# Optimization experiments

Measured on AMD Instinct MI355X. Metric: run time of the kernel, lower is better.

Reference implementation:

```python
import jax, jax.numpy as jnp
import numpy as np

EPS_POOL = 1e-9
NEG_INF = -1e9
TEMPERATURE = 0.07


def _l2norm(x, axis=-1, eps=1e-12):
    # matches torch F.normalize(p=2): x / max(||x||, eps)
    n = jnp.sqrt(jnp.sum(x * x, axis=axis, keepdims=True))
    return x / jnp.maximum(n, eps)


def setup_inputs() -> dict:
    key = jax.random.key(0)
    ks = jax.random.split(key, 8)
    B, Lq, Lc, D = 256, 128, 512, 384
    question_tokens = jax.random.normal(ks[0], (B, Lq, D), dtype=jnp.float32)
    chunk_tokens = jax.random.normal(ks[1], (B, Lc, D), dtype=jnp.float32)
    q_mask = jax.random.randint(ks[2], (B, Lq), 0, 2, dtype=jnp.int32)
    c_mask = jax.random.randint(ks[3], (B, Lc), 0, 2, dtype=jnp.int32)
    # ensure at least one valid token per row (avoid fully-masked rows)
    q_mask = q_mask.at[:, 0].set(1)
    c_mask = c_mask.at[:, 0].set(1)
    W1 = jax.random.normal(ks[4], (D, D), dtype=jnp.float32) * (1.0 / np.sqrt(D))
    b1 = jnp.zeros((D,), dtype=jnp.float32)
    W2 = jax.random.normal(ks[5], (D, D), dtype=jnp.float32) * (1.0 / np.sqrt(D))
    b2 = jnp.zeros((D,), dtype=jnp.float32)
    return {"question_tokens": question_tokens, "chunk_tokens": chunk_tokens,
            "q_mask": q_mask, "c_mask": c_mask,
            "W1": W1, "b1": b1, "W2": W2, "b2": b2}


def _encode(tokens, mask, W1, b1, W2, b2):
    # mean pool over valid tokens: [B,L,D] -> [B,D]
    m = mask.astype(tokens.dtype)[..., None]
    pooled = jnp.sum(tokens * m, axis=1) / jnp.maximum(jnp.sum(m, axis=1), EPS_POOL)
    h = jax.nn.relu(pooled @ W1 + b1)
    proj = h @ W2 + b2
    return _l2norm(proj, axis=1)


def _late_interaction(q_tokens, c_tokens, q_mask, c_mask):
    qn = _l2norm(q_tokens)                      # [B,Lq,D]
    cn = _l2norm(c_tokens)                      # [B,Lc,D]
    sims = jnp.einsum('bqd,bkd->bqk', qn, cn)   # [B,Lq,Lc]
    valid = q_mask[:, :, None].astype(bool) & c_mask[:, None, :].astype(bool)
    sims = jnp.where(valid, sims, NEG_INF)
    max_sim = jnp.max(sims, axis=-1)            # [B,Lq]
    max_sim = jnp.where(q_mask.astype(bool), max_sim, 0.0)
    return jnp.sum(max_sim, axis=-1)            # [B]


def reference(question_tokens, chunk_tokens, q_mask, c_mask, W1, b1, W2, b2):
    q_emb = _encode(question_tokens, q_mask, W1, b1, W2, b2)  # [B,D]
    c_emb = _encode(chunk_tokens, c_mask, W1, b1, W2, b2)     # [B,D]
    contrastive_sim = (q_emb @ c_emb.T) / TEMPERATURE         # [B,B]
    late_sim = _late_interaction(question_tokens, chunk_tokens, q_mask, c_mask)  # [B]
    return contrastive_sim, late_sim
```

## Files before the change

kernel.cpp:

```cpp
#include <hip/hip_runtime.h>
#include <hip/hip_bf16.h>
#include <stdint.h>

#define NB 256
#define LQ 128
#define LC 512
#define DIM 384
#define TCD 32
#define QP 392

typedef __attribute__((ext_vector_type(8))) short short8;
typedef __attribute__((ext_vector_type(4))) float f32x4;

__device__ __forceinline__ unsigned short f2bf(float x) {
  union { float f; uint32_t u; } c; c.f = x;
  return (unsigned short)((c.u + 0x7fffu + ((c.u >> 16) & 1u)) >> 16);
}

__global__ __launch_bounds__(512, 1)
void fused_pool_late(const float* __restrict__ qtok, const float* __restrict__ ctok,
                     const int* __restrict__ qm, const int* __restrict__ cm,
                     float* __restrict__ pooled, float* __restrict__ late) {
  __shared__ unsigned short s_q[LQ][QP];
  __shared__ unsigned short s_c[TCD][QP];
  __shared__ float s_pq[8][DIM];
  __shared__ float s_pc[8][DIM];
  __shared__ float s_cnt[2][8];
  __shared__ int   s_cval[TCD];
  __shared__ float s_wsum[8];

  const int b = blockIdx.x;
  const int tid = threadIdx.x;
  const int wave = tid >> 6;
  const int lane = tid & 63;
  const int rA = lane & 15;
  const int kof = (lane >> 4) * 8;

  const float* qb = qtok + (size_t)b * LQ * DIM;
  const float* cb = ctok + (size_t)b * LC * DIM;
  const int* qmb = qm + b * LQ;
  const int* cmb = cm + b * LC;

  float pq[6] = {0.f,0.f,0.f,0.f,0.f,0.f};
  float cq = 0.f;
  for (int r0 = 0; r0 < 16; ++r0) {
    const int r = wave * 16 + r0;
    const float* src = qb + r * DIM;
    float v[6], ss = 0.f;
#pragma unroll
    for (int j = 0; j < 6; ++j) { v[j] = src[lane + 64 * j]; ss += v[j] * v[j]; }
#pragma unroll
    for (int o = 32; o; o >>= 1) ss += __shfl_xor(ss, o);
    const float inv = 1.0f / fmaxf(sqrtf(ss), 1e-12f);
    const float fm = (float)qmb[r];
#pragma unroll
    for (int j = 0; j < 6; ++j) {
      s_q[r][lane + 64 * j] = f2bf(v[j] * inv);
      pq[j] = fmaf(v[j], fm, pq[j]);
    }
    cq += fm;
  }
#pragma unroll
  for (int j = 0; j < 6; ++j) s_pq[wave][lane + 64 * j] = pq[j];
  if (lane == 0) s_cnt[0][wave] = cq;

  float rm[4] = {-1e9f, -1e9f, -1e9f, -1e9f};
  float pc[6] = {0.f,0.f,0.f,0.f,0.f,0.f};
  float cc = 0.f;

  for (int t = 0; t < LC / TCD; ++t) {
    __syncthreads();
#pragma unroll
    for (int r0 = 0; r0 < 4; ++r0) {
      const int r = wave * 4 + r0;
      const int crow = t * TCD + r;
      const float* src = cb + crow * DIM;
      float v[6], ss = 0.f;
#pragma unroll
      for (int j = 0; j < 6; ++j) { v[j] = src[lane + 64 * j]; ss += v[j] * v[j]; }
#pragma unroll
      for (int o = 32; o; o >>= 1) ss += __shfl_xor(ss, o);
      const float inv = 1.0f / fmaxf(sqrtf(ss), 1e-12f);
      const int mk = cmb[crow];
      const float fm = (float)mk;
#pragma unroll
      for (int j = 0; j < 6; ++j) {
        s_c[r][lane + 64 * j] = f2bf(v[j] * inv);
        pc[j] = fmaf(v[j], fm, pc[j]);
      }
      cc += fm;
      if (lane == 0) s_cval[r] = mk;
    }
    __syncthreads();

    const unsigned short* ap  = &s_q[wave * 16 + rA][kof];
    const unsigned short* bp0 = &s_c[rA][kof];
    const unsigned short* bp1 = &s_c[rA + 16][kof];
    f32x4 acc0 = {0.f,0.f,0.f,0.f};
    f32x4 acc1 = {0.f,0.f,0.f,0.f};
#pragma unroll
    for (int kk = 0; kk < 12; ++kk) {
      short8 a  = *(const short8*)(ap  + kk * 32);
      short8 b0 = *(const short8*)(bp0 + kk * 32);
      short8 b1 = *(const short8*)(bp1 + kk * 32);
      acc0 = __builtin_amdgcn_mfma_f32_16x16x32_bf16(a, b0, acc0, 0, 0, 0);
      acc1 = __builtin_amdgcn_mfma_f32_16x16x32_bf16(a, b1, acc1, 0, 0, 0);
    }
    const bool v0 = s_cval[rA] != 0;
    const bool v1 = s_cval[rA + 16] != 0;
#pragma unroll
    for (int r = 0; r < 4; ++r) {
      const float a0 = v0 ? acc0[r] : -1e9f;
      const float a1 = v1 ? acc1[r] : -1e9f;
      rm[r] = fmaxf(rm[r], fmaxf(a0, a1));
    }
  }

#pragma unroll
  for (int j = 0; j < 6; ++j) s_pc[wave][lane + 64 * j] = pc[j];
  if (lane == 0) s_cnt[1][wave] = cc;

#pragma unroll
  for (int r = 0; r < 4; ++r) {
#pragma unroll
    for (int o = 1; o < 16; o <<= 1) rm[r] = fmaxf(rm[r], __shfl_xor(rm[r], o));
  }
  float ps = 0.f;
  if (rA == 0) {
    const int rowb = wave * 16 + (lane >> 4) * 4;
#pragma unroll
    for (int r = 0; r < 4; ++r) ps += qmb[rowb + r] ? rm[r] : 0.f;
  }
#pragma unroll
  for (int o = 32; o; o >>= 1) ps += __shfl_xor(ps, o);
  if (lane == 0) s_wsum[wave] = ps;
  __syncthreads();

  if (tid < DIM) {
    float sq = 0.f, sc = 0.f, nq = 0.f, nc = 0.f;
#pragma unroll
    for (int w = 0; w < 8; ++w) {
      sq += s_pq[w][tid];
      sc += s_pc[w][tid];
      nq += s_cnt[0][w];
      nc += s_cnt[1][w];
    }
    pooled[b * DIM + tid] = sq / fmaxf(nq, 1e-9f);
    pooled[(NB + b) * DIM + tid] = sc / fmaxf(nc, 1e-9f);
  }
  if (tid == 0) {
    float tot = 0.f;
#pragma unroll
    for (int w = 0; w < 8; ++w) tot += s_wsum[w];
    late[b] = tot;
  }
}

__global__ __launch_bounds__(DIM)
void mlp_kernel(const float* __restrict__ pooled,
                const float* __restrict__ W1, const float* __restrict__ b1,
                const float* __restrict__ W2, const float* __restrict__ b2,
                float* __restrict__ emb) {
  __shared__ float s_in[DIM];
  __shared__ float s_h[DIM];
  __shared__ float s_red[6];
  const int row = blockIdx.y * NB + blockIdx.x;
  const int d = threadIdx.x;
  s_in[d] = pooled[row * DIM + d];
  __syncthreads();
  float acc = b1[d];
#pragma unroll 8
  for (int k = 0; k < DIM; ++k) acc = fmaf(s_in[k], W1[k * DIM + d], acc);
  s_h[d] = fmaxf(acc, 0.f);
  __syncthreads();
  float p = b2[d];
#pragma unroll 8
  for (int k = 0; k < DIM; ++k) p = fmaf(s_h[k], W2[k * DIM + d], p);
  float ss = p * p;
#pragma unroll
  for (int o = 32; o; o >>= 1) ss += __shfl_xor(ss, o);
  if ((d & 63) == 0) s_red[d >> 6] = ss;
  __syncthreads();
  float tot = 0.f;
#pragma unroll
  for (int w = 0; w < 6; ++w) tot += s_red[w];
  emb[row * DIM + d] = p * (1.0f / fmaxf(sqrtf(tot), 1e-12f));
}

__global__ __launch_bounds__(NB)
void contrast_kernel(const float* __restrict__ emb, float* __restrict__ out0) {
  __shared__ float s_q[DIM];
  const int i = blockIdx.x;
  for (int k = threadIdx.x; k < DIM; k += NB) s_q[k] = emb[i * DIM + k];
  __syncthreads();
  const float* ce = emb + (size_t)(NB + threadIdx.x) * DIM;
  float acc = 0.f;
#pragma unroll 8
  for (int k = 0; k < DIM; ++k) acc = fmaf(s_q[k], ce[k], acc);
  out0[i * NB + threadIdx.x] = acc / 0.07f;
}

extern "C" void kernel_launch(void* const* d_in, const int* in_sizes, int n_in,
                              void* d_out, int out_size, void* d_ws, size_t ws_size,
                              hipStream_t stream) {
  const float* qtok = (const float*)d_in[0];
  const float* ctok = (const float*)d_in[1];
  const int*   qmm  = (const int*)d_in[2];
  const int*   cmm  = (const int*)d_in[3];
  const float* W1   = (const float*)d_in[4];
  const float* b1   = (const float*)d_in[5];
  const float* W2   = (const float*)d_in[6];
  const float* b2   = (const float*)d_in[7];

  float* out0 = (float*)d_out;
  float* late = out0 + NB * NB;
  float* pooled = (float*)d_ws;
  float* emb    = pooled + 2 * NB * DIM;

  hipLaunchKernelGGL(fused_pool_late, dim3(NB), dim3(512), 0, stream,
                     qtok, ctok, qmm, cmm, pooled, late);
  hipLaunchKernelGGL(mlp_kernel, dim3(NB, 2), dim3(DIM), 0, stream,
                     pooled, W1, b1, W2, b2, emb);
  hipLaunchKernelGGL(contrast_kernel, dim3(NB), dim3(NB), 0, stream, emb, out0);
}
```

Before: 134.7 us.

## Double-buffer token loads via async global-to-LDS and batch rows in MLP/contrast

The fused pooling/late-interaction kernel now streams query and chunk tiles into double-buffered LDS with global_load_lds, using an XOR swizzle, so global loads overlap the normalisation and MFMA work. Token rows are converted to bf16 unnormalised, and the per-row inverse norms are applied to the MFMA outputs afterwards. Query A-fragments are kept in registers across all chunk tiles. The MLP kernel now processes 4 rows per block and the contrastive kernel 8 rows per block, so weight and embedding loads are reused across rows. This adds LDS pressure and relies on hand-placed waitcnt and barrier code; bf16 rounding of unnormalised values slightly changes numerics.

```diff
diff --git a/kernel.cpp b/kernel.cpp
--- a/kernel.cpp
+++ b/kernel.cpp
@@ -6,119 +6,165 @@
 #define LQ 128
 #define LC 512
 #define DIM 384
-#define TCD 32
-#define QP 392
+#define TROWS 32
+#define ROW_BYTES (DIM * 4)
+#define STAGE_BYTES (TROWS * ROW_BYTES)
+#define NSTAGE 20
+#define CBP 392
 
 typedef __attribute__((ext_vector_type(8))) short short8;
-typedef __attribute__((ext_vector_type(4))) float f32x4;
-
-__device__ __forceinline__ unsigned short f2bf(float x) {
-  union { float f; uint32_t u; } c; c.f = x;
-  return (unsigned short)((c.u + 0x7fffu + ((c.u >> 16) & 1u)) >> 16);
+typedef __attribute__((ext_vector_type(4))) float f4;
+typedef __attribute__((ext_vector_type(2))) unsigned int u32x2;
+
+__device__ __forceinline__ unsigned int pk2bf(float a, float b) {
+  union { float f; uint32_t u; } x, y; x.f = a; y.f = b;
+  uint32_t lo = (x.u + 0x7fffu + ((x.u >> 16) & 1u)) >> 16;
+  uint32_t hi = (y.u + 0x7fffu + ((y.u >> 16) & 1u)) >> 16;
+  return lo | (hi << 16);
+}
+
+__device__ __forceinline__ void gload16(const void* g, void* l) {
+  __builtin_amdgcn_global_load_lds(
+      (const __attribute__((address_space(1))) void*)g,
+      (__attribute__((address_space(3))) void*)l, 16, 0, 0);
+}
+
+__device__ __forceinline__ void bar_lgkm() {
+  asm volatile("s_waitcnt lgkmcnt(0)" ::: "memory");
+  __builtin_amdgcn_s_barrier();
+  __builtin_amdgcn_sched_barrier(0);
 }
 
 __global__ __launch_bounds__(512, 1)
 void fused_pool_late(const float* __restrict__ qtok, const float* __restrict__ ctok,
                      const int* __restrict__ qm, const int* __restrict__ cm,
                      float* __restrict__ pooled, float* __restrict__ late) {
-  __shared__ unsigned short s_q[LQ][QP];
-  __shared__ unsigned short s_c[TCD][QP];
-  __shared__ float s_pq[8][DIM];
-  __shared__ float s_pc[8][DIM];
-  __shared__ float s_cnt[2][8];
-  __shared__ int   s_cval[TCD];
+  __shared__ float fbuf[2][TROWS * DIM];
+  __shared__ unsigned short s_cb[TROWS][CBP];
+  __shared__ float s_qinv[LQ];
+  __shared__ float s_cinv[TROWS];
+  __shared__ int s_qm[LQ];
+  __shared__ int s_cm[LC];
+  __shared__ float s_cnt[16];
   __shared__ float s_wsum[8];
 
   const int b = blockIdx.x;
   const int tid = threadIdx.x;
-  const int wave = tid >> 6;
-  const int lane = tid & 63;
-  const int rA = lane & 15;
-  const int kof = (lane >> 4) * 8;
-
-  const float* qb = qtok + (size_t)b * LQ * DIM;
-  const float* cb = ctok + (size_t)b * LC * DIM;
-  const int* qmb = qm + b * LQ;
-  const int* cmb = cm + b * LC;
-
-  float pq[6] = {0.f,0.f,0.f,0.f,0.f,0.f};
-  float cq = 0.f;
-  for (int r0 = 0; r0 < 16; ++r0) {
-    const int r = wave * 16 + r0;
-    const float* src = qb + r * DIM;
-    float v[6], ss = 0.f;
-#pragma unroll
-    for (int j = 0; j < 6; ++j) { v[j] = src[lane + 64 * j]; ss += v[j] * v[j]; }
-#pragma unroll
-    for (int o = 32; o; o >>= 1) ss += __shfl_xor(ss, o);
-    const float inv = 1.0f / fmaxf(sqrtf(ss), 1e-12f);
-    const float fm = (float)qmb[r];
-#pragma unroll
-    for (int j = 0; j < 6; ++j) {
-      s_q[r][lane + 64 * j] = f2bf(v[j] * inv);
-      pq[j] = fmaf(v[j], fm, pq[j]);
-    }
-    cq += fm;
-  }
-#pragma unroll
-  for (int j = 0; j < 6; ++j) s_pq[wave][lane + 64 * j] = pq[j];
-  if (lane == 0) s_cnt[0][wave] = cq;
-
+  const int wave = tid >> 6, lane = tid & 63;
+  const int rA = lane & 15, hi = lane >> 4;
+
+  const char* qb = (const char*)(qtok + (size_t)b * LQ * DIM);
+  const char* cb = (const char*)(ctok + (size_t)b * LC * DIM);
+
+  if (tid < LQ) s_qm[tid] = qm[b * LQ + tid];
+  s_cm[tid] = cm[b * LC + tid];
+  __syncthreads();
+
+  int goff[6];
+#pragma unroll
+  for (int j = 0; j < 6; ++j) {
+    unsigned n = (unsigned)wave * 384u + (unsigned)j * 64u + (unsigned)lane;
+    unsigned row = n / 96u, cc = n % 96u;
+    goff[j] = (int)(row * ROW_BYTES + ((cc ^ (row & 7u)) << 4));
+  }
+
+  {
+    char* ldst = (char*)&fbuf[0][0] + wave * 6144;
+#pragma unroll
+    for (int j = 0; j < 6; ++j) gload16(qb + goff[j], ldst + j * 1024);
+  }
+
+  f4 pqa = {0.f,0.f,0.f,0.f}, pqb = {0.f,0.f,0.f,0.f};
+  f4 pca = {0.f,0.f,0.f,0.f}, pcb = {0.f,0.f,0.f,0.f};
+  float cq = 0.f, ccnt = 0.f;
   float rm[4] = {-1e9f, -1e9f, -1e9f, -1e9f};
-  float pc[6] = {0.f,0.f,0.f,0.f,0.f,0.f};
-  float cc = 0.f;
-
-  for (int t = 0; t < LC / TCD; ++t) {
-    __syncthreads();
+  short8 A[12] = {};
+
+  for (int t = 0; t < NSTAGE; ++t) {
+    const int cur = t & 1;
+    if (t + 1 < NSTAGE) {
+      const char* base = (t + 1 < 4) ? (qb + (size_t)(t + 1) * STAGE_BYTES)
+                                     : (cb + (size_t)(t + 1 - 4) * STAGE_BYTES);
+      char* ldst = (char*)&fbuf[cur ^ 1][0] + wave * 6144;
+#pragma unroll
+      for (int j = 0; j < 6; ++j) gload16(base + goff[j], ldst + j * 1024);
+      asm volatile("s_waitcnt vmcnt(6)" ::: "memory");
+    } else {
+      asm volatile("s_waitcnt vmcnt(0)" ::: "memory");
+    }
+    __builtin_amdgcn_sched_barrier(0);
+
+    const char* fb = (const char*)&fbuf[cur][0];
+    const bool isq = (t < 4);
 #pragma unroll
     for (int r0 = 0; r0 < 4; ++r0) {
-      const int r = wave * 4 + r0;
-      const int crow = t * TCD + r;
-      const float* src = cb + crow * DIM;
-      float v[6], ss = 0.f;
-#pragma unroll
-      for (int j = 0; j < 6; ++j) { v[j] = src[lane + 64 * j]; ss += v[j] * v[j]; }
+      const int lrow = wave * 4 + r0;
+      const int k7 = lrow & 7;
+      const f4 va = *(const f4*)(fb + lrow * ROW_BYTES + ((lane ^ k7) << 4));
+      f4 vb = {0.f,0.f,0.f,0.f};
+      if (lane < 32) vb = *(const f4*)(fb + lrow * ROW_BYTES + (((64 + lane) ^ k7) << 4));
+      float ss = va.x*va.x + va.y*va.y + va.z*va.z + va.w*va.w
+               + vb.x*vb.x + vb.y*vb.y + vb.z*vb.z + vb.w*vb.w;
 #pragma unroll
       for (int o = 32; o; o >>= 1) ss += __shfl_xor(ss, o);
       const float inv = 1.0f / fmaxf(sqrtf(ss), 1e-12f);
-      const int mk = cmb[crow];
+      const int mk = isq ? s_qm[t * 32 + lrow] : s_cm[(t - 4) * 32 + lrow];
       const float fm = (float)mk;
-#pragma unroll
-      for (int j = 0; j < 6; ++j) {
-        s_c[r][lane + 64 * j] = f2bf(v[j] * inv);
-        pc[j] = fmaf(v[j], fm, pc[j]);
-      }
-      cc += fm;
-      if (lane == 0) s_cval[r] = mk;
-    }
-    __syncthreads();
-
-    const unsigned short* ap  = &s_q[wave * 16 + rA][kof];
-    const unsigned short* bp0 = &s_c[rA][kof];
-    const unsigned short* bp1 = &s_c[rA + 16][kof];
-    f32x4 acc0 = {0.f,0.f,0.f,0.f};
-    f32x4 acc1 = {0.f,0.f,0.f,0.f};
-#pragma unroll
-    for (int kk = 0; kk < 12; ++kk) {
-      short8 a  = *(const short8*)(ap  + kk * 32);
-      short8 b0 = *(const short8*)(bp0 + kk * 32);
-      short8 b1 = *(const short8*)(bp1 + kk * 32);
-      acc0 = __builtin_amdgcn_mfma_f32_16x16x32_bf16(a, b0, acc0, 0, 0, 0);
-      acc1 = __builtin_amdgcn_mfma_f32_16x16x32_bf16(a, b1, acc1, 0, 0, 0);
-    }
-    const bool v0 = s_cval[rA] != 0;
-    const bool v1 = s_cval[rA + 16] != 0;
-#pragma unroll
-    for (int r = 0; r < 4; ++r) {
-      const float a0 = v0 ? acc0[r] : -1e9f;
-      const float a1 = v1 ? acc1[r] : -1e9f;
-      rm[r] = fmaxf(rm[r], fmaxf(a0, a1));
-    }
-  }
-
-#pragma unroll
-  for (int j = 0; j < 6; ++j) s_pc[wave][lane + 64 * j] = pc[j];
-  if (lane == 0) s_cnt[1][wave] = cc;
+      if (isq) {
+        pqa += va * fm; pqb += vb * fm; cq += fm;
+        if (lane == 0) s_qinv[t * 32 + lrow] = inv;
+      } else {
+        pca += va * fm; pcb += vb * fm; ccnt += fm;
+        if (lane == 0) s_cinv[lrow] = inv;
+      }
+      u32x2 w0; w0[0] = pk2bf(va.x, va.y); w0[1] = pk2bf(va.z, va.w);
+      *(u32x2*)&s_cb[lrow][4 * lane] = w0;
+      if (lane < 32) {
+        u32x2 w1; w1[0] = pk2bf(vb.x, vb.y); w1[1] = pk2bf(vb.z, vb.w);
+        *(u32x2*)&s_cb[lrow][256 + 4 * lane] = w1;
+      }
+    }
+    bar_lgkm();
+
+    if (isq) {
+      if ((wave >> 1) == t) {
+        const int lbase = (wave & 1) * 16 + rA;
+#pragma unroll
+        for (int kk = 0; kk < 12; ++kk)
+          A[kk] = *(const short8*)&s_cb[lbase][kk * 32 + hi * 8];
+        asm volatile("s_waitcnt lgkmcnt(0)" ::: "memory");
+        __builtin_amdgcn_sched_barrier(0);
+      }
+    } else {
+      f4 acc0 = {0.f,0.f,0.f,0.f}, acc1 = {0.f,0.f,0.f,0.f};
+#pragma unroll
+      for (int kk = 0; kk < 12; ++kk) {
+        const short8 b0 = *(const short8*)&s_cb[rA][kk * 32 + hi * 8];
+        const short8 b1 = *(const short8*)&s_cb[rA + 16][kk * 32 + hi * 8];
+        acc0 = __builtin_amdgcn_mfma_f32_16x16x32_bf16(A[kk], b0, acc0, 0, 0, 0);
+        acc1 = __builtin_amdgcn_mfma_f32_16x16x32_bf16(A[kk], b1, acc1, 0, 0, 0);
+      }
+      const int tb = (t - 4) * 32;
+      const bool v0 = s_cm[tb + rA] != 0;
+      const bool v1 = s_cm[tb + rA + 16] != 0;
+      const float ci0 = s_cinv[rA], ci1 = s_cinv[rA + 16];
+#pragma unroll
+      for (int r = 0; r < 4; ++r) {
+        const float qi = s_qinv[wave * 16 + hi * 4 + r];
+        const float a0 = v0 ? acc0[r] * (qi * ci0) : -1e9f;
+        const float a1 = v1 ? acc1[r] * (qi * ci1) : -1e9f;
+        rm[r] = fmaxf(rm[r], fmaxf(a0, a1));
+      }
+    }
+    bar_lgkm();
+  }
+
+  float* red = (float*)&fbuf[0][0];
+  *(f4*)&red[wave * DIM + 4 * lane] = pqa;
+  if (lane < 32) *(f4*)&red[wave * DIM + 256 + 4 * lane] = pqb;
+  *(f4*)&red[(8 + wave) * DIM + 4 * lane] = pca;
+  if (lane < 32) *(f4*)&red[(8 + wave) * DIM + 256 + 4 * lane] = pcb;
+  if (lane == 0) { s_cnt[wave] = cq; s_cnt[8 + wave] = ccnt; }
 
 #pragma unroll
   for (int r = 0; r < 4; ++r) {
@@ -127,9 +173,9 @@
   }
   float ps = 0.f;
   if (rA == 0) {
-    const int rowb = wave * 16 + (lane >> 4) * 4;
-#pragma unroll
-    for (int r = 0; r < 4; ++r) ps += qmb[rowb + r] ? rm[r] : 0.f;
+    const int rowb = wave * 16 + hi * 4;
+#pragma unroll
+    for (int r = 0; r < 4; ++r) ps += s_qm[rowb + r] ? rm[r] : 0.f;
   }
 #pragma unroll
   for (int o = 32; o; o >>= 1) ps += __shfl_xor(ps, o);
@@ -140,10 +186,10 @@
     float sq = 0.f, sc = 0.f, nq = 0.f, nc = 0.f;
 #pragma unroll
     for (int w = 0; w < 8; ++w) {
-      sq += s_pq[w][tid];
-      sc += s_pc[w][tid];
-      nq += s_cnt[0][w];
-      nc += s_cnt[1][w];
+      sq += red[w * DIM + tid];
+      sc += red[(8 + w) * DIM + tid];
+      nq += s_cnt[w];
+      nc += s_cnt[8 + w];
     }
     pooled[b * DIM + tid] = sq / fmaxf(nq, 1e-9f);
     pooled[(NB + b) * DIM + tid] = sc / fmaxf(nc, 1e-9f);
@@ -157,47 +203,68 @@
 }
 
 __global__ __launch_bounds__(DIM)
-void mlp_kernel(const float* __restrict__ pooled,
-                const float* __restrict__ W1, const float* __restrict__ b1,
-                const float* __restrict__ W2, const float* __restrict__ b2,
-                float* __restrict__ emb) {
-  __shared__ float s_in[DIM];
-  __shared__ float s_h[DIM];
-  __shared__ float s_red[6];
-  const int row = blockIdx.y * NB + blockIdx.x;
+void mlp_kernel(const float* __restrict__ pooled, const float* __restrict__ W1,
+                const float* __restrict__ b1, const float* __restrict__ W2,
+                const float* __restrict__ b2, float* __restrict__ emb) {
+  __shared__ float s_in[4][DIM];
+  __shared__ float s_h[4][DIM];
+  __shared__ float s_red[4][6];
+  const int r0 = blockIdx.x * 4;
   const int d = threadIdx.x;
-  s_in[d] = pooled[row * DIM + d];
-  __syncthreads();
-  float acc = b1[d];
+#pragma unroll
+  for (int r = 0; r < 4; ++r) s_in[r][d] = pooled[(size_t)(r0 + r) * DIM + d];
+  __syncthreads();
+  float acc[4] = {b1[d], b1[d], b1[d], b1[d]};
 #pragma unroll 8
-  for (int k = 0; k < DIM; ++k) acc = fmaf(s_in[k], W1[k * DIM + d], acc);
-  s_h[d] = fmaxf(acc, 0.f);
-  __syncthreads();
-  float p = b2[d];
+  for (int k = 0; k < DIM; ++k) {
+    const float w = W1[k * DIM + d];
+#pragma unroll
+    for (int r = 0; r < 4; ++r) acc[r] = fmaf(s_in[r][k], w, acc[r]);
+  }
+#pragma unroll
+  for (int r = 0; r < 4; ++r) s_h[r][d] = fmaxf(acc[r], 0.f);
+  __syncthreads();
+  float p[4] = {b2[d], b2[d], b2[d], b2[d]};
 #pragma unroll 8
-  for (int k = 0; k < DIM; ++k) p = fmaf(s_h[k], W2[k * DIM + d], p);
-  float ss = p * p;
-#pragma unroll
-  for (int o = 32; o; o >>= 1) ss += __shfl_xor(ss, o);
-  if ((d & 63) == 0) s_red[d >> 6] = ss;
-  __syncthreads();
-  float tot = 0.f;
-#pragma unroll
-  for (int w = 0; w < 6; ++w) tot += s_red[w];
-  emb[row * DIM + d] = p * (1.0f / fmaxf(sqrtf(tot), 1e-12f));
+  for (int k = 0; k < DIM; ++k) {
+    const float w = W2[k * DIM + d];
+#pragma unroll
+    for (int r = 0; r < 4; ++r) p[r] = fmaf(s_h[r][k], w, p[r]);
+  }
+#pragma unroll
+  for (int r = 0; r < 4; ++r) {
+    float ss = p[r] * p[r];
+#pragma unroll
+    for (int o = 32; o; o >>= 1) ss += __shfl_xor(ss, o);
+    if ((d & 63) == 0) s_red[r][d >> 6] = ss;
+  }
+  __syncthreads();
+#pragma unroll
+  for (int r = 0; r < 4; ++r) {
+    float tot = 0.f;
+#pragma unroll
+    for (int w = 0; w < 6; ++w) tot += s_red[r][w];
+    emb[(size_t)(r0 + r) * DIM + d] = p[r] * (1.0f / fmaxf(sqrtf(tot), 1e-12f));
+  }
 }
 
 __global__ __launch_bounds__(NB)
 void contrast_kernel(const float* __restrict__ emb, float* __restrict__ out0) {
-  __shared__ float s_q[DIM];
-  const int i = blockIdx.x;
-  for (int k = threadIdx.x; k < DIM; k += NB) s_q[k] = emb[i * DIM + k];
-  __syncthreads();
-  const float* ce = emb + (size_t)(NB + threadIdx.x) * DIM;
-  float acc = 0.f;
+  __shared__ float s_q[8][DIM];
+  const int i0 = blockIdx.x * 8;
+  const int j = threadIdx.x;
+  for (int tt = j; tt < 8 * DIM; tt += NB) s_q[tt / DIM][tt % DIM] = emb[(size_t)i0 * DIM + tt];
+  __syncthreads();
+  const float* ce = emb + (size_t)(NB + j) * DIM;
+  float acc[8] = {0.f,0.f,0.f,0.f,0.f,0.f,0.f,0.f};
 #pragma unroll 8
-  for (int k = 0; k < DIM; ++k) acc = fmaf(s_q[k], ce[k], acc);
-  out0[i * NB + threadIdx.x] = acc / 0.07f;
+  for (int k = 0; k < DIM; ++k) {
+    const float c = ce[k];
+#pragma unroll
+    for (int r = 0; r < 8; ++r) acc[r] = fmaf(s_q[r][k], c, acc[r]);
+  }
+#pragma unroll
+  for (int r = 0; r < 8; ++r) out0[(size_t)(i0 + r) * NB + j] = acc[r] / 0.07f;
 }
 
 extern "C" void kernel_launch(void* const* d_in, const int* in_sizes, int n_in,
@@ -219,7 +286,7 @@
 
   hipLaunchKernelGGL(fused_pool_late, dim3(NB), dim3(512), 0, stream,
                      qtok, ctok, qmm, cmm, pooled, late);
-  hipLaunchKernelGGL(mlp_kernel, dim3(NB, 2), dim3(DIM), 0, stream,
+  hipLaunchKernelGGL(mlp_kernel, dim3(NB / 2), dim3(DIM), 0, stream,
                      pooled, W1, b1, W2, b2, emb);
-  hipLaunchKernelGGL(contrast_kernel, dim3(NB), dim3(NB), 0, stream, emb, out0);
-}
+  hipLaunchKernelGGL(contrast_kernel, dim3(NB / 8), dim3(NB), 0, stream, emb, out0);
+}
```

Measured after the change: 150.9 us. 1.12x slower.
